# Optimization experiments

Measured on AMD Instinct MI355X. Metric: run time of the kernel, lower is better.

Reference implementation:

```python
import jax, jax.numpy as jnp
import numpy as np

D = 1024      # dim_input
H = 16        # n_heads
DH = 64       # dim_inner
S = 1024      # current_seq
M = 1024      # pre_seq (memory)
B = 2         # batch
SCALE = 1.0 / np.sqrt(DH)


def _rel_shift(x):
    # x: [S, J, B, H]; Transformer-XL relative shift
    s, j = x.shape[0], x.shape[1]
    zero = jnp.zeros((s, 1) + x.shape[2:], x.dtype)
    x = jnp.concatenate([zero, x], axis=1)            # [S, J+1, B, H]
    x = x.reshape((j + 1, s) + x.shape[2:])[1:]        # [J, S, B, H]
    return x.reshape((s, j) + x.shape[2:])             # [S, J, B, H]


def setup_inputs() -> dict:
    key = jax.random.key(0)
    ks = jax.random.split(key, 9)
    std = 1.0 / np.sqrt(D)
    return {
        "multi_head_input": jax.random.normal(ks[0], (S, B, D), jnp.float32),
        "position_emb": jax.random.normal(ks[1], (S + M, D), jnp.float32),
        "memory": jax.random.normal(ks[2], (M, B, D), jnp.float32),
        "u": jax.random.normal(ks[3], (H, DH), jnp.float32) * 0.02,
        "v": jax.random.normal(ks[4], (H, DH), jnp.float32) * 0.02,
        "W_kv": jax.random.normal(ks[5], (D, 2 * H * DH), jnp.float32) * std,
        "W_q": jax.random.normal(ks[6], (D, H * DH), jnp.float32) * std,
        "W_pos": jax.random.normal(ks[7], (D, H * DH), jnp.float32) * std,
        "W_out": jax.random.normal(ks[8], (H * DH, D), jnp.float32) * std,
    }


def reference(multi_head_input, position_emb, memory, u, v, W_kv, W_q, W_pos, W_out):
    s = multi_head_input.shape[0]
    m = memory.shape[0]
    b = multi_head_input.shape[1]
    x_mem = jnp.concatenate([memory, multi_head_input], axis=0)   # [M+S, B, D]
    kv = x_mem @ W_kv                                              # [M+S, B, 2*H*DH]
    k, val = jnp.split(kv, 2, axis=-1)
    k = k.reshape(m + s, b, H, DH)
    val = val.reshape(m + s, b, H, DH)
    q = (multi_head_input @ W_q).reshape(s, b, H, DH)              # [S, B, H, DH]

    # content term: (q + u) . k
    content = jnp.einsum('ibhd,jbhd->ijbh', q + u, k)              # [S, M+S, B, H]
    # position term: (q + v) . r, then rel_shift
    r = (position_emb @ W_pos).reshape(m + s, H, DH)               # [M+S, H, DH]
    pos = jnp.einsum('ibhd,jhd->ijbh', q + v, r)                   # [S, M+S, B, H]
    pos = _rel_shift(pos)

    attn = jax.nn.softmax((content + pos) * SCALE, axis=1)         # [S, M+S, B, H]
    out = jnp.einsum('ijbh,jbhd->ibhd', attn, val).reshape(s, b, H * DH)
    return out @ W_out                                             # [S, B, D]
```

## Files before the change

kernel.cpp:

```cpp
#include <hip/hip_runtime.h>
#include <hip/hip_bf16.h>
#include <hip/hip_fp16.h>
#include <math.h>

#define D    1024
#define H    16
#define DH   64
#define S    1024
#define M    1024
#define B    2
#define J    2048
#define SCALE 0.125f

typedef __attribute__((ext_vector_type(8))) short        bf16x8;
typedef __attribute__((ext_vector_type(4))) short        s16x4;
typedef __attribute__((ext_vector_type(8))) _Float16     h16x8;
typedef __attribute__((ext_vector_type(8))) unsigned short us8;
typedef __attribute__((ext_vector_type(4))) float        f32x4;

__device__ __forceinline__ short f2bs(float f) {
    __hip_bfloat16 t = __float2bfloat16(f);
    short r; __builtin_memcpy(&r, &t, 2); return r;
}
__device__ __forceinline__ unsigned short f2bf_fast(float f) {
    unsigned int u; __builtin_memcpy(&u, &f, 4);
    return (unsigned short)((u + 0x8000u) >> 16);
}

__device__ __forceinline__ void g2l16(const short* g, short* l) {
    __builtin_amdgcn_global_load_lds(
        (const __attribute__((address_space(1))) unsigned int*)g,
        (__attribute__((address_space(3))) unsigned int*)l, 16, 0, 0);
}

__global__ __launch_bounds__(256)
void prep(const float* __restrict__ mem, const float* __restrict__ x,
          const float* __restrict__ pemb,
          const float* __restrict__ Wkv, const float* __restrict__ Wq,
          const float* __restrict__ Wpos, const float* __restrict__ Wout,
          short* __restrict__ a_bf, short* __restrict__ p_bf,
          short* __restrict__ wkvt, short* __restrict__ wqt,
          short* __restrict__ wpt,  short* __restrict__ wot)
{
    __shared__ float t[64][65];
    int blk = blockIdx.x;
    const int tid = threadIdx.x;
    if (blk < 6144) {
        const int idx = (blk * 256 + tid) * 4;
        const int TWO_M = 2 * 1024 * 1024;
        float4 v; short* dst;
        if (idx < TWO_M)          { v = *(const float4*)(mem  + idx);           dst = a_bf + idx; }
        else if (idx < 2 * TWO_M) { v = *(const float4*)(x    + idx - TWO_M);   dst = a_bf + idx; }
        else                      { v = *(const float4*)(pemb + idx - 2*TWO_M); dst = p_bf + idx - 2*TWO_M; }
        s16x4 o = { f2bs(v.x), f2bs(v.y), f2bs(v.z), f2bs(v.w) };
        *(s16x4*)dst = o;
        return;
    }
    blk -= 6144;
    const float* src; short* dst; int N, t0;
    if (blk < 512)       { src = Wkv;  dst = wkvt; N = 2048; t0 = blk; }
    else if (blk < 768)  { src = Wq;   dst = wqt;  N = 1024; t0 = blk - 512; }
    else if (blk < 1024) { src = Wpos; dst = wpt;  N = 1024; t0 = blk - 768; }
    else                 { src = Wout; dst = wot;  N = 1024; t0 = blk - 1024; }
    const int ntn = N >> 6;
    const int k0 = (t0 / ntn) * 64, n0 = (t0 % ntn) * 64;
    #pragma unroll
    for (int e = tid; e < 4096; e += 256) {
        int r = e >> 6, c = e & 63;
        t[r][c] = src[(size_t)(k0 + r) * N + n0 + c];
    }
    __syncthreads();
    #pragma unroll
    for (int e = tid; e < 4096; e += 256) {
        int nr = e >> 6, kc = e & 63;
        dst[(size_t)(n0 + nr) * 1024 + k0 + kc] = f2bs(t[kc][nr]);
    }
}

__device__ __forceinline__ void gemm_core(const short* __restrict__ A,
                                          const short* __restrict__ Bt,
                                          short* As, short* Bs,
                                          int bm0, int bn0, int tid,
                                          f32x4 acc[4][4])
{
    const int w    = tid >> 6;
    const int wy   = w >> 1, wx = w & 1;
    const int lane = tid & 63;
    const int lm   = lane & 15;
    const int lq   = lane >> 4;

    for (int k0 = 0; k0 < 1024; k0 += 64) {
        const short* Ab = A  + (size_t)bm0 * 1024 + k0;
        const short* Bb = Bt + (size_t)bn0 * 1024 + k0;
        #pragma unroll
        for (int t = 0; t < 4; ++t) {
            int s = t * 256 + tid;
            int r = s >> 3, c = s & 7;
            int cg = c ^ (r & 7);
            g2l16(Ab + r * 1024 + cg * 8, As + s * 8);
            g2l16(Bb + r * 1024 + cg * 8, Bs + s * 8);
        }
        __syncthreads();
        #pragma unroll
        for (int kk = 0; kk < 2; ++kk) {
            bf16x8 af[4], bg[4];
            #pragma unroll
            for (int r4 = 0; r4 < 4; ++r4) {
                int ar = wy * 64 + r4 * 16 + lm;
                int kc = kk * 4 + lq;
                af[r4] = *(const bf16x8*)(As + ((ar << 3) + (kc ^ (ar & 7))) * 8);
            }
            #pragma unroll
            for (int c4 = 0; c4 < 4; ++c4) {
                int br = wx * 64 + c4 * 16 + lm;
                int kc = kk * 4 + lq;
                bg[c4] = *(const bf16x8*)(Bs + ((br << 3) + (kc ^ (br & 7))) * 8);
            }
            #pragma unroll
            for (int r4 = 0; r4 < 4; ++r4)
                #pragma unroll
                for (int c4 = 0; c4 < 4; ++c4)
                    acc[r4][c4] = __builtin_amdgcn_mfma_f32_16x16x32_bf16(
                        af[r4], bg[c4], acc[r4][c4], 0, 0, 0);
        }
        __syncthreads();
    }
}

__global__ __launch_bounds__(256)
void proj_fused(const short* __restrict__ a_bf, const short* __restrict__ p_bf,
                const short* __restrict__ wkvt, const short* __restrict__ wqt,
                const short* __restrict__ wpt,
                short* __restrict__ k_bf, short* __restrict__ vt_bf,
                short* __restrict__ qu_bf, short* __restrict__ qv_bf,
                short* __restrict__ r_bf,
                const float* __restrict__ uvec, const float* __restrict__ vvec)
{
    __shared__ __align__(16) short As[128 * 64];
    __shared__ __align__(16) short Bs[128 * 64];

    int blk = blockIdx.x;
    int mode, bx, by;
    const short *A, *Bt;
    if (blk < 512)      { bx = blk & 15; by = blk >> 4;
                          if (bx >= 8) { mode = 4; A = wkvt; Bt = a_bf; }
                          else         { mode = 0; A = a_bf; Bt = wkvt; } }
    else if (blk < 640) { int b2 = blk - 512; mode = 1; bx = b2 & 7; by = b2 >> 3;
                          A = a_bf + (size_t)2048 * 1024; Bt = wqt; }
    else                { int b3 = blk - 640; mode = 2; bx = b3 & 7; by = b3 >> 3;
                          A = p_bf; Bt = wpt; }
    const int bn0 = (mode == 4) ? by * 128 : bx * 128;
    const int bm0 = (mode == 4) ? bx * 128 : by * 128;
    const int tid = threadIdx.x;
    const int w = tid >> 6, wy = w >> 1, wx = w & 1;
    const int lane = tid & 63, lm = lane & 15, lq = lane >> 4;

    f32x4 acc[4][4];
    #pragma unroll
    for (int r = 0; r < 4; ++r)
        #pragma unroll
        for (int c = 0; c < 4; ++c) acc[r][c] = (f32x4){0.f, 0.f, 0.f, 0.f};

    gemm_core(A, Bt, As, Bs, bm0, bn0, tid, acc);

    #pragma unroll
    for (int r4 = 0; r4 < 4; ++r4) {
        #pragma unroll
        for (int c4 = 0; c4 < 4; ++c4) {
            const int n = bn0 + wx * 64 + c4 * 16 + lm;
            float ubias = 0.f, vbias = 0.f;
            if (mode == 1) { ubias = uvec[n]; vbias = vvec[n]; }
            #pragma unroll
            for (int reg = 0; reg < 4; ++reg) {
                const int m = bm0 + wy * 64 + r4 * 16 + lq * 4 + reg;
                const float val = acc[r4][c4][reg];
                if (mode == 0) {
                    int j = m >> 1, b = m & 1;
                    int h = n >> 6, d = n & 63;
                    k_bf[(((size_t)b * H + h) * J + j) * DH + d] = f2bs(val);
                } else if (mode == 4) {
                    int n2 = m - 1024, h = n2 >> 6, d = n2 & 63;
                    int j = n >> 1, b = n & 1;
                    vt_bf[(((size_t)b * H + h) * DH + d) * J + j] = f2bs(val);
                } else if (mode == 1) {
                    int i = m >> 1, b = m & 1;
                    int h = n >> 6, d = n & 63;
                    size_t o = (((size_t)b * H + h) * S + i) * DH + d;
                    qu_bf[o] = f2bs((val + ubias) * SCALE);
                    qv_bf[o] = f2bs((val + vbias) * SCALE);
                } else {
                    int h = n >> 6, d = n & 63;
                    r_bf[((size_t)h * J + m) * DH + d] = f2bs(val);
                }
            }
        }
    }
}

__global__ __launch_bounds__(256)
void gemm_out(const short* __restrict__ A, const short* __restrict__ Bt,
              float* __restrict__ out)
{
    __shared__ __align__(16) short As[128 * 64];
    __shared__ __align__(16) short Bs[128 * 64];
    const int bn0 = blockIdx.x * 128, bm0 = blockIdx.y * 128;
    const int tid = threadIdx.x;
    const int w = tid >> 6, wy = w >> 1, wx = w & 1;
    const int lane = tid & 63, lm = lane & 15, lq = lane >> 4;

    f32x4 acc[4][4];
    #pragma unroll
    for (int r = 0; r < 4; ++r)
        #pragma unroll
        for (int c = 0; c < 4; ++c) acc[r][c] = (f32x4){0.f, 0.f, 0.f, 0.f};

    gemm_core(A, Bt, As, Bs, bm0, bn0, tid, acc);

    #pragma unroll
    for (int r4 = 0; r4 < 4; ++r4)
        #pragma unroll
        for (int c4 = 0; c4 < 4; ++c4) {
            const int n = bn0 + wx * 64 + c4 * 16 + lm;
            #pragma unroll
            for (int reg = 0; reg < 4; ++reg) {
                const int m = bm0 + wy * 64 + r4 * 16 + lq * 4 + reg;
                out[(size_t)m * 1024 + n] = acc[r4][c4][reg];
            }
        }
}

__device__ __forceinline__ int sidx(int m, int c) {
    return (m << 10) + (c ^ (m << 3));
}

__global__ __launch_bounds__(512)
void attn_mfma(const short* __restrict__ qu_bf, const short* __restrict__ qv_bf,
               const short* __restrict__ k_bf,  const short* __restrict__ vt_bf,
               const short* __restrict__ r_bf,
               float* __restrict__ opart, float* __restrict__ ml)
{
    __shared__ unsigned short sc[32 * 1024];
    __half* sch = (__half*)sc;
    float*  scF = (float*)sc;

    const int bh  = blockIdx.x;
    const int it  = blockIdx.y;
    const int jh  = blockIdx.z;
    const int i0  = it * 32;
    const int cbeg = jh << 10, cend = cbeg + 1024;
    const int h   = bh & (H - 1);
    const int tid = threadIdx.x;
    const int w    = tid >> 6;
    const int lane = tid & 63;
    const int lm   = lane & 15;
    const int lq   = lane >> 4;
    const int slot = (it * 32 + bh) * 2 + jh;

    const short* qup0 = qu_bf + ((size_t)(bh * S + i0 + lm)) * DH + lq * 8;
    const short* qup1 = qup0 + 16 * DH;
    bf16x8 au00 = *(const bf16x8*)qup0,        au01 = *(const bf16x8*)(qup0 + 32);
    bf16x8 au10 = *(const bf16x8*)qup1,        au11 = *(const bf16x8*)(qup1 + 32);
    const short* qvp0 = qv_bf + ((size_t)(bh * S + i0 + lm)) * DH + lq * 8;
    const short* qvp1 = qvp0 + 16 * DH;
    bf16x8 av00 = *(const bf16x8*)qvp0,        av01 = *(const bf16x8*)(qvp0 + 32);
    bf16x8 av10 = *(const bf16x8*)qvp1,        av11 = *(const bf16x8*)(qvp1 + 32);
    int r1a = i0 + 1 + lm;  if (r1a > S - 1) r1a = S - 1;
    int r1b = i0 + 17 + lm; if (r1b > S - 1) r1b = S - 1;
    const short* qwp0 = qv_bf + ((size_t)(bh * S + r1a)) * DH + lq * 8;
    const short* qwp1 = qv_bf + ((size_t)(bh * S + r1b)) * DH + lq * 8;
    bf16x8 aw00 = *(const bf16x8*)qwp0,        aw01 = *(const bf16x8*)(qwp0 + 32);
    bf16x8 aw10 = *(const bf16x8*)qwp1,        aw11 = *(const bf16x8*)(qwp1 + 32);

    if (tid < 32) {
        int hole = i0 + tid + 1025;
        if (hole >= cbeg && hole < cend) sc[sidx(tid, hole - cbeg)] = 0;
    }

    const short* rbase = r_bf + (size_t)h * J * DH;

    {
        int tmp = cbeg + 977 - i0;
        int tlo = tmp > 0 ? ((tmp + 15) >> 4) : 0;
        int thi = (cend + 1022 - i0) >> 4; if (thi > 127) thi = 127;
        for (int t = tlo + w; t <= thi; t += 8) {
            const short* rp = rbase + (size_t)(t * 16 + lm) * DH + lq * 8;
            bf16x8 b0 = *(const bf16x8*)rp, b1 = *(const bf16x8*)(rp + 32);
            f32x4 c0 = {0.f,0.f,0.f,0.f}, c1 = {0.f,0.f,0.f,0.f};
            c0 = __builtin_amdgcn_mfma_f32_16x16x32_bf16(av00, b0, c0, 0, 0, 0);
            c1 = __builtin_amdgcn_mfma_f32_16x16x32_bf16(av10, b0, c1, 0, 0, 0);
            c0 = __builtin_amdgcn_mfma_f32_16x16x32_bf16(av01, b1, c0, 0, 0, 0);
            c1 = __builtin_amdgcn_mfma_f32_16x16x32_bf16(av11, b1, c1, 0, 0, 0);
            int cb = i0 + t * 16 + lm - 1023 - cbeg;
            int base = i0 + 16 * t - 1023;
            if (base >= cbeg && base + 46 < cend) {
                #pragma unroll
                for (int r = 0; r < 4; ++r) {
                    int m0 = lq * 4 + r, m1 = m0 + 16;
                    sch[sidx(m0, cb + m0)] = __float2half(c0[r]);
                    sch[sidx(m1, cb + m1)] = __float2half(c1[r]);
                }
            } else {
                #pragma unroll
                for (int r = 0; r < 4; ++r) {
                    int m0 = lq * 4 + r, m1 = m0 + 16;
                    int cA = cb + m0, cB = cb + m1;
                    if (cA >= 0 && cA < 1024) sch[sidx(m0, cA)] = __float2half(c0[r]);
                    if (cB >= 0 && cB < 1024) sch[sidx(m1, cB)] = __float2half(c1[r]);
                }
            }
        }
    }

    {
        int tmpw = cbeg - 1072 - i0;
        int tlw = tmpw > 0 ? ((tmpw + 15) >> 4) : 0;
        int thw = (cend - 1027 - i0) >> 4; if (thw > 127) thw = 127;
        for (int t = tlw + w; t <= thw; t += 8) {
            const short* rp = rbase + (size_t)(t * 16 + lm) * DH + lq * 8;
            bf16x8 b0 = *(const bf16x8*)rp, b1 = *(const bf16x8*)(rp + 32);
            f32x4 c0 = {0.f,0.f,0.f,0.f}, c1 = {0.f,0.f,0.f,0.f};
            c0 = __builtin_amdgcn_mfma_f32_16x16x32_bf16(aw00, b0, c0, 0, 0, 0);
            c1 = __builtin_amdgcn_mfma_f32_16x16x32_bf16(aw10, b0, c1, 0, 0, 0);
            c0 = __builtin_amdgcn_mfma_f32_16x16x32_bf16(aw01, b1, c0, 0, 0, 0);
            c1 = __builtin_amdgcn_mfma_f32_16x16x32_bf16(aw11, b1, c1, 0, 0, 0);
            int cb = i0 + t * 16 + lm + 1026 - cbeg;
            int base = i0 + 16 * t + 1026;
            if (base >= cbeg && base + 46 < cend) {
                #pragma unroll
                for (int r = 0; r < 4; ++r) {
                    int m0 = lq * 4 + r, m1 = m0 + 16;
                    sch[sidx(m0, cb + m0)] = __float2half(c0[r]);
                    sch[sidx(m1, cb + m1)] = __float2half(c1[r]);
                }
            } else {
                #pragma unroll
                for (int r = 0; r < 4; ++r) {
                    int m0 = lq * 4 + r, m1 = m0 + 16;
                    int cA = cb + m0, cB = cb + m1;
                    if (cA >= 0 && cA < 1024) sch[sidx(m0, cA)] = __float2half(c0[r]);
                    if (cB >= 0 && cB < 1024) sch[sidx(m1, cB)] = __float2half(c1[r]);
                }
            }
        }
    }

    const short* kbase = k_bf + (size_t)bh * J * DH;
    int tc0 = jh * 64 + w + 8 * ((it) & 7);
    int tc1 = jh * 64 + w + 8 * ((1 + it) & 7);
    const short* kp0 = kbase + (size_t)(tc0 * 16 + lm) * DH + lq * 8;
    const short* kp1 = kbase + (size_t)(tc1 * 16 + lm) * DH + lq * 8;
    bf16x8 kb0 = *(const bf16x8*)kp0, kb1 = *(const bf16x8*)(kp0 + 32);
    bf16x8 kb2 = *(const bf16x8*)kp1, kb3 = *(const bf16x8*)(kp1 + 32);
    __syncthreads();

    #pragma unroll 1
    for (int g = 0; g < 8; g += 2) {
        int t0 = jh * 64 + w + 8 * ((g + it) & 7);
        int t1 = jh * 64 + w + 8 * ((g + 1 + it) & 7);
        bf16x8 nb0, nb1, nb2, nb3;
        if (g + 2 < 8) {
            int u0 = jh * 64 + w + 8 * ((g + 2 + it) & 7);
            int u1 = jh * 64 + w + 8 * ((g + 3 + it) & 7);
            const short* np0 = kbase + (size_t)(u0 * 16 + lm) * DH + lq * 8;
            const short* np1 = kbase + (size_t)(u1 * 16 + lm) * DH + lq * 8;
            nb0 = *(const bf16x8*)np0; nb1 = *(const bf16x8*)(np0 + 32);
            nb2 = *(const bf16x8*)np1; nb3 = *(const bf16x8*)(np1 + 32);
        }
        int lc0 = t0 * 16 + lm - cbeg;
        int lc1 = t1 * 16 + lm - cbeg;
        f32x4 c0, c1, c2, c3;
        #pragma unroll
        for (int r = 0; r < 4; ++r) {
            c0[r] = __half2float(sch[sidx(lq * 4 + r, lc0)]);
            c1[r] = __half2float(sch[sidx(16 + lq * 4 + r, lc0)]);
            c2[r] = __half2float(sch[sidx(lq * 4 + r, lc1)]);
            c3[r] = __half2float(sch[sidx(16 + lq * 4 + r, lc1)]);
        }
        c0 = __builtin_amdgcn_mfma_f32_16x16x32_bf16(au00, kb0, c0, 0, 0, 0);
        c1 = __builtin_amdgcn_mfma_f32_16x16x32_bf16(au10, kb0, c1, 0, 0, 0);
        c2 = __builtin_amdgcn_mfma_f32_16x16x32_bf16(au00, kb2, c2, 0, 0, 0);
        c3 = __builtin_amdgcn_mfma_f32_16x16x32_bf16(au10, kb2, c3, 0, 0, 0);
        c0 = __builtin_amdgcn_mfma_f32_16x16x32_bf16(au01, kb1, c0, 0, 0, 0);
        c1 = __builtin_amdgcn_mfma_f32_16x16x32_bf16(au11, kb1, c1, 0, 0, 0);
        c2 = __builtin_amdgcn_mfma_f32_16x16x32_bf16(au01, kb3, c2, 0, 0, 0);
        c3 = __builtin_amdgcn_mfma_f32_16x16x32_bf16(au11, kb3, c3, 0, 0, 0);
        #pragma unroll
        for (int r = 0; r < 4; ++r) {
            sch[sidx(lq * 4 + r, lc0)]      = __float2half(c0[r]);
            sch[sidx(16 + lq * 4 + r, lc0)] = __float2half(c1[r]);
            sch[sidx(lq * 4 + r, lc1)]      = __float2half(c2[r]);
            sch[sidx(16 + lq * 4 + r, lc1)] = __float2half(c3[r]);
        }
        kb0 = nb0; kb1 = nb1; kb2 = nb2; kb3 = nb3;
    }

    const int dslice = w & 3, jq = w >> 2;
    const short* vtb = vt_bf + ((size_t)bh * DH + dslice * 16 + lm) * J + cbeg + jq * 512;
    bf16x8 cv0, cv1, cv2, cv3;
    {
        int j0 = (it & 3) * 128;
        cv0 = *(const bf16x8*)(vtb + j0 +  0 + lq * 8);
        cv1 = *(const bf16x8*)(vtb + j0 + 32 + lq * 8);
        cv2 = *(const bf16x8*)(vtb + j0 + 64 + lq * 8);
        cv3 = *(const bf16x8*)(vtb + j0 + 96 + lq * 8);
    }
    __syncthreads();

    {
        const int row = tid >> 4;
        const int cw  = (tid & 15) * 8;
        float ssum = 0.f;
        #pragma unroll
        for (int c = cw; c < 1024; c += 128) {
            int idx = sidx(row, c);
            h16x8 v = *(const h16x8*)(sc + idx);
            us8 e;
            #pragma unroll
            for (int k = 0; k < 8; ++k) {
                float ex = __builtin_amdgcn_exp2f((float)v[k] * 1.44269504f);
                ssum += ex;
                e[k] = f2bf_fast(ex);
            }
            *(us8*)(sc + idx) = e;
        }
        #pragma unroll
        for (int off = 1; off < 16; off <<= 1) ssum += __shfl_xor(ssum, off);
        if ((tid & 15) == 0) {
            ml[(size_t)slot * 64 + row * 2]     = 0.f;
            ml[(size_t)slot * 64 + row * 2 + 1] = ssum;
        }
    }
    __syncthreads();

    f32x4 pa0 = {0.f,0.f,0.f,0.f}, pa1 = {0.f,0.f,0.f,0.f};
    f32x4 pa2 = {0.f,0.f,0.f,0.f}, pa3 = {0.f,0.f,0.f,0.f};
    f32x4 pb0 = {0.f,0.f,0.f,0.f}, pb1 = {0.f,0.f,0.f,0.f};
    f32x4 pb2 = {0.f,0.f,0.f,0.f}, pb3 = {0.f,0.f,0.f,0.f};
    #pragma unroll 1
    for (int jo0 = 0; jo0 < 4; ++jo0) {
        bf16x8 nv0, nv1, nv2, nv3;
        if (jo0 < 3) {
            int jn = ((jo0 + 1 + it) & 3) * 128;
            nv0 = *(const bf16x8*)(vtb + jn +  0 + lq * 8);
            nv1 = *(const bf16x8*)(vtb + jn + 32 + lq * 8);
            nv2 = *(const bf16x8*)(vtb + jn + 64 + lq * 8);
            nv3 = *(const bf16x8*)(vtb + jn + 96 + lq * 8);
        }
        int j0 = ((jo0 + it) & 3) * 128;
        int lb = jq * 512 + j0;
        bf16x8 a0 = *(const bf16x8*)(sc + sidx(lm, lb +  0 + lq * 8));
        bf16x8 a1 = *(const bf16x8*)(sc + sidx(lm, lb + 32 + lq * 8));
        bf16x8 a2 = *(const bf16x8*)(sc + sidx(lm, lb + 64 + lq * 8));
        bf16x8 a3 = *(const bf16x8*)(sc + sidx(lm, lb + 96 + lq * 8));
        bf16x8 c0 = *(const bf16x8*)(sc + sidx(16 + lm, lb +  0 + lq * 8));
        bf16x8 c1 = *(const bf16x8*)(sc + sidx(16 + lm, lb + 32 + lq * 8));
        bf16x8 c2 = *(const bf16x8*)(sc + sidx(16 + lm, lb + 64 + lq * 8));
        bf16x8 c3 = *(const bf16x8*)(sc + sidx(16 + lm, lb + 96 + lq * 8));
        pa0 = __builtin_amdgcn_mfma_f32_16x16x32_bf16(a0, cv0, pa0, 0, 0, 0);
        pb0 = __builtin_amdgcn_mfma_f32_16x16x32_bf16(c0, cv0, pb0, 0, 0, 0);
        pa1 = __builtin_amdgcn_mfma_f32_16x16x32_bf16(a1, cv1, pa1, 0, 0, 0);
        pb1 = __builtin_amdgcn_mfma_f32_16x16x32_bf16(c1, cv1, pb1, 0, 0, 0);
        pa2 = __builtin_amdgcn_mfma_f32_16x16x32_bf16(a2, cv2, pa2, 0, 0, 0);
        pb2 = __builtin_amdgcn_mfma_f32_16x16x32_bf16(c2, cv2, pb2, 0, 0, 0);
        pa3 = __builtin_amdgcn_mfma_f32_16x16x32_bf16(a3, cv3, pa3, 0, 0, 0);
        pb3 = __builtin_amdgcn_mfma_f32_16x16x32_bf16(c3, cv3, pb3, 0, 0, 0);
        if (jo0 < 3) { cv0 = nv0; cv1 = nv1; cv2 = nv2; cv3 = nv3; }
    }
    __syncthreads();

    #pragma unroll
    for (int r = 0; r < 4; ++r) {
        int m0 = lq * 4 + r, m1 = m0 + 16;
        scF[jq * 2048 + m0 * 64 + dslice * 16 + lm] = pa0[r] + pa1[r] + pa2[r] + pa3[r];
        scF[jq * 2048 + m1 * 64 + dslice * 16 + lm] = pb0[r] + pb1[r] + pb2[r] + pb3[r];
    }
    __syncthreads();

    float* op = opart + (size_t)slot * 2048;
    #pragma unroll
    for (int e = tid; e < 2048; e += 512)
        op[e] = scF[e] + scF[2048 + e];
}

__global__ __launch_bounds__(256)
void attn_combine(const float* __restrict__ opart, const float* __restrict__ ml,
                  short* __restrict__ o_bf)
{
    const int blk = blockIdx.x;
    const int it = blk >> 5, bh = blk & 31;
    const int h = bh & 15, b = bh >> 4;
    __shared__ float wgt[32][2];
    const int tid = threadIdx.x;
    if (tid < 32) {
        float m0 = ml[(size_t)(blk * 2 + 0) * 64 + tid * 2];
        float l0 = ml[(size_t)(blk * 2 + 0) * 64 + tid * 2 + 1];
        float m1 = ml[(size_t)(blk * 2 + 1) * 64 + tid * 2];
        float l1 = ml[(size_t)(blk * 2 + 1) * 64 + tid * 2 + 1];
        float mx = fmaxf(m0, m1);
        float e0 = __expf(m0 - mx), e1 = __expf(m1 - mx);
        float inv = 1.0f / (e0 * l0 + e1 * l1);
        wgt[tid][0] = e0 * inv;
        wgt[tid][1] = e1 * inv;
    }
    __syncthreads();
    const float* p0 = opart + (size_t)(blk * 2 + 0) * 2048;
    const float* p1 = opart + (size_t)(blk * 2 + 1) * 2048;
    #pragma unroll
    for (int e = tid; e < 2048; e += 256) {
        int m = e >> 6, d = e & 63;
        float val = p0[e] * wgt[m][0] + p1[e] * wgt[m][1];
        o_bf[((size_t)(it * 32 + m) * B + b) * (H * DH) + h * DH + d] = f2bs(val);
    }
}

extern "C" void kernel_launch(void* const* d_in, const int* in_sizes, int n_in,
                              void* d_out, int out_size, void* d_ws, size_t ws_size,
                              hipStream_t stream)
{
    const float* x    = (const float*)d_in[0];
    const float* pemb = (const float*)d_in[1];
    const float* mem  = (const float*)d_in[2];
    const float* u    = (const float*)d_in[3];
    const float* v    = (const float*)d_in[4];
    const float* Wkv  = (const float*)d_in[5];
    const float* Wq   = (const float*)d_in[6];
    const float* Wpos = (const float*)d_in[7];
    const float* Wout = (const float*)d_in[8];
    float* out = (float*)d_out;

    char* p = (char*)d_ws;
    short* a_bf  = (short*)p; p += (size_t)4096 * 1024 * 2;
    short* p_bf  = (short*)p; p += (size_t)2048 * 1024 * 2;
    short* wkvt  = (short*)p; p += (size_t)2048 * 1024 * 2;
    short* wqt   = (short*)p; p += (size_t)1024 * 1024 * 2;
    short* wpt   = (short*)p; p += (size_t)1024 * 1024 * 2;
    short* wot   = (short*)p; p += (size_t)1024 * 1024 * 2;
    short* k_bf  = (short*)p; p += (size_t)B * H * J * DH * 2;
    short* vt_bf = (short*)p; p += (size_t)B * H * J * DH * 2;
    short* qu_bf = (short*)p; p += (size_t)B * H * S * DH * 2;
    short* qv_bf = (short*)p; p += (size_t)B * H * S * DH * 2;
    short* r_bf  = (short*)p; p += (size_t)H * J * DH * 2;
    short* o_bf  = (short*)p;

    float* opart = (float*)d_ws;
    float* ml    = (float*)((char*)d_ws + (size_t)16 * 1024 * 1024);

    prep<<<7424, 256, 0, stream>>>(mem, x, pemb, Wkv, Wq, Wpos, Wout,
                                   a_bf, p_bf, wkvt, wqt, wpt, wot);
    proj_fused<<<768, 256, 0, stream>>>(a_bf, p_bf, wkvt, wqt, wpt,
                                        k_bf, vt_bf, qu_bf, qv_bf, r_bf, u, v);
    attn_mfma<<<dim3(B * H, S / 32, 2), 512, 0, stream>>>(
        qu_bf, qv_bf, k_bf, vt_bf, r_bf, opart, ml);
    attn_combine<<<(S / 32) * B * H, 256, 0, stream>>>(opart, ml, o_bf);
    gemm_out<<<dim3(8, 16), 256, 0, stream>>>(o_bf, wot, out);
}
```

Before: 293.9 us.

## Fuse exp into PV MFMA loop with per-wave column ownership

Instead of a separate pass that exponentiates the score tile in shared memory and writes it back as bf16, each wave now takes its own 128-column slice. It exponentiates the fp16 scores in registers and feeds them straight into the P·V MFMAs, with each wave covering all four d-slices. This removes an LDS read-modify-write pass and one barrier. In exchange the per-wave partial outputs must be reduced across 8 waves through LDS, and row sums are written per wave and summed in the combine kernel, which is simplified because the row max is always zero.

Measured after the change: 295.5 us. No clear change (+0.6%).

```diff
diff --git a/kernel.cpp b/kernel.cpp
--- a/kernel.cpp
+++ b/kernel.cpp
@@ -237,9 +237,9 @@
 void attn_mfma(const short* __restrict__ qu_bf, const short* __restrict__ qv_bf,
                const short* __restrict__ k_bf,  const short* __restrict__ vt_bf,
                const short* __restrict__ r_bf,
-               float* __restrict__ opart, float* __restrict__ ml)
-{
-    __shared__ unsigned short sc[32 * 1024];
+               float* __restrict__ opart, float* __restrict__ lsum)
+{
+    __shared__ __align__(16) unsigned short sc[32 * 1024];
     __half* sch = (__half*)sc;
     float*  scF = (float*)sc;
 
@@ -393,114 +393,90 @@
         }
         kb0 = nb0; kb1 = nb1; kb2 = nb2; kb3 = nb3;
     }
-
-    const int dslice = w & 3, jq = w >> 2;
-    const short* vtb = vt_bf + ((size_t)bh * DH + dslice * 16 + lm) * J + cbeg + jq * 512;
-    bf16x8 cv0, cv1, cv2, cv3;
+    __syncthreads();
+
+    f32x4 acc[4][2];
+    #pragma unroll
+    for (int ds = 0; ds < 4; ++ds) {
+        acc[ds][0] = (f32x4){0.f, 0.f, 0.f, 0.f};
+        acc[ds][1] = (f32x4){0.f, 0.f, 0.f, 0.f};
+    }
+    float rs0 = 0.f, rs1 = 0.f;
+    #pragma unroll 1
+    for (int c = 0; c < 4; ++c) {
+        int jb = w * 128 + ((c + it) & 3) * 32;
+        h16x8 ra0 = *(const h16x8*)(sc + sidx(lm, jb + lq * 8));
+        h16x8 ra1 = *(const h16x8*)(sc + sidx(16 + lm, jb + lq * 8));
+        bf16x8 bv[4];
+        #pragma unroll
+        for (int ds = 0; ds < 4; ++ds)
+            bv[ds] = *(const bf16x8*)(vt_bf +
+                ((size_t)bh * DH + ds * 16 + lm) * J + cbeg + jb + lq * 8);
+        us8 pa, pb;
+        #pragma unroll
+        for (int k = 0; k < 8; ++k) {
+            float e0 = __builtin_amdgcn_exp2f((float)ra0[k] * 1.44269504f);
+            float e1 = __builtin_amdgcn_exp2f((float)ra1[k] * 1.44269504f);
+            rs0 += e0; rs1 += e1;
+            pa[k] = f2bf_fast(e0);
+            pb[k] = f2bf_fast(e1);
+        }
+        bf16x8 a0, a1;
+        __builtin_memcpy(&a0, &pa, 16);
+        __builtin_memcpy(&a1, &pb, 16);
+        #pragma unroll
+        for (int ds = 0; ds < 4; ++ds) {
+            acc[ds][0] = __builtin_amdgcn_mfma_f32_16x16x32_bf16(a0, bv[ds], acc[ds][0], 0, 0, 0);
+            acc[ds][1] = __builtin_amdgcn_mfma_f32_16x16x32_bf16(a1, bv[ds], acc[ds][1], 0, 0, 0);
+        }
+    }
+    rs0 += __shfl_xor(rs0, 16); rs0 += __shfl_xor(rs0, 32);
+    rs1 += __shfl_xor(rs1, 16); rs1 += __shfl_xor(rs1, 32);
+    if (lq == 0) {
+        lsum[(size_t)slot * 256 + w * 32 + lm]      = rs0;
+        lsum[(size_t)slot * 256 + w * 32 + 16 + lm] = rs1;
+    }
+    __syncthreads();
+
+    #pragma unroll
+    for (int ds = 0; ds < 4; ++ds)
+        #pragma unroll
+        for (int r = 0; r < 4; ++r) {
+            int m0 = lq * 4 + r, m1 = m0 + 16;
+            scF[w * 2048 + m0 * 64 + ds * 16 + lm] = acc[ds][0][r];
+            scF[w * 2048 + m1 * 64 + ds * 16 + lm] = acc[ds][1][r];
+        }
+    __syncthreads();
+
     {
-        int j0 = (it & 3) * 128;
-        cv0 = *(const bf16x8*)(vtb + j0 +  0 + lq * 8);
-        cv1 = *(const bf16x8*)(vtb + j0 + 32 + lq * 8);
-        cv2 = *(const bf16x8*)(vtb + j0 + 64 + lq * 8);
-        cv3 = *(const bf16x8*)(vtb + j0 + 96 + lq * 8);
-    }
-    __syncthreads();
-
-    {
-        const int row = tid >> 4;
-        const int cw  = (tid & 15) * 8;
-        float ssum = 0.f;
-        #pragma unroll
-        for (int c = cw; c < 1024; c += 128) {
-            int idx = sidx(row, c);
-            h16x8 v = *(const h16x8*)(sc + idx);
-            us8 e;
-            #pragma unroll
-            for (int k = 0; k < 8; ++k) {
-                float ex = __builtin_amdgcn_exp2f((float)v[k] * 1.44269504f);
-                ssum += ex;
-                e[k] = f2bf_fast(ex);
-            }
-            *(us8*)(sc + idx) = e;
-        }
-        #pragma unroll
-        for (int off = 1; off < 16; off <<= 1) ssum += __shfl_xor(ssum, off);
-        if ((tid & 15) == 0) {
-            ml[(size_t)slot * 64 + row * 2]     = 0.f;
-            ml[(size_t)slot * 64 + row * 2 + 1] = ssum;
-        }
-    }
-    __syncthreads();
-
-    f32x4 pa0 = {0.f,0.f,0.f,0.f}, pa1 = {0.f,0.f,0.f,0.f};
-    f32x4 pa2 = {0.f,0.f,0.f,0.f}, pa3 = {0.f,0.f,0.f,0.f};
-    f32x4 pb0 = {0.f,0.f,0.f,0.f}, pb1 = {0.f,0.f,0.f,0.f};
-    f32x4 pb2 = {0.f,0.f,0.f,0.f}, pb3 = {0.f,0.f,0.f,0.f};
-    #pragma unroll 1
-    for (int jo0 = 0; jo0 < 4; ++jo0) {
-        bf16x8 nv0, nv1, nv2, nv3;
-        if (jo0 < 3) {
-            int jn = ((jo0 + 1 + it) & 3) * 128;
-            nv0 = *(const bf16x8*)(vtb + jn +  0 + lq * 8);
-            nv1 = *(const bf16x8*)(vtb + jn + 32 + lq * 8);
-            nv2 = *(const bf16x8*)(vtb + jn + 64 + lq * 8);
-            nv3 = *(const bf16x8*)(vtb + jn + 96 + lq * 8);
-        }
-        int j0 = ((jo0 + it) & 3) * 128;
-        int lb = jq * 512 + j0;
-        bf16x8 a0 = *(const bf16x8*)(sc + sidx(lm, lb +  0 + lq * 8));
-        bf16x8 a1 = *(const bf16x8*)(sc + sidx(lm, lb + 32 + lq * 8));
-        bf16x8 a2 = *(const bf16x8*)(sc + sidx(lm, lb + 64 + lq * 8));
-        bf16x8 a3 = *(const bf16x8*)(sc + sidx(lm, lb + 96 + lq * 8));
-        bf16x8 c0 = *(const bf16x8*)(sc + sidx(16 + lm, lb +  0 + lq * 8));
-        bf16x8 c1 = *(const bf16x8*)(sc + sidx(16 + lm, lb + 32 + lq * 8));
-        bf16x8 c2 = *(const bf16x8*)(sc + sidx(16 + lm, lb + 64 + lq * 8));
-        bf16x8 c3 = *(const bf16x8*)(sc + sidx(16 + lm, lb + 96 + lq * 8));
-        pa0 = __builtin_amdgcn_mfma_f32_16x16x32_bf16(a0, cv0, pa0, 0, 0, 0);
-        pb0 = __builtin_amdgcn_mfma_f32_16x16x32_bf16(c0, cv0, pb0, 0, 0, 0);
-        pa1 = __builtin_amdgcn_mfma_f32_16x16x32_bf16(a1, cv1, pa1, 0, 0, 0);
-        pb1 = __builtin_amdgcn_mfma_f32_16x16x32_bf16(c1, cv1, pb1, 0, 0, 0);
-        pa2 = __builtin_amdgcn_mfma_f32_16x16x32_bf16(a2, cv2, pa2, 0, 0, 0);
-        pb2 = __builtin_amdgcn_mfma_f32_16x16x32_bf16(c2, cv2, pb2, 0, 0, 0);
-        pa3 = __builtin_amdgcn_mfma_f32_16x16x32_bf16(a3, cv3, pa3, 0, 0, 0);
-        pb3 = __builtin_amdgcn_mfma_f32_16x16x32_bf16(c3, cv3, pb3, 0, 0, 0);
-        if (jo0 < 3) { cv0 = nv0; cv1 = nv1; cv2 = nv2; cv3 = nv3; }
-    }
-    __syncthreads();
-
-    #pragma unroll
-    for (int r = 0; r < 4; ++r) {
-        int m0 = lq * 4 + r, m1 = m0 + 16;
-        scF[jq * 2048 + m0 * 64 + dslice * 16 + lm] = pa0[r] + pa1[r] + pa2[r] + pa3[r];
-        scF[jq * 2048 + m1 * 64 + dslice * 16 + lm] = pb0[r] + pb1[r] + pb2[r] + pb3[r];
-    }
-    __syncthreads();
-
-    float* op = opart + (size_t)slot * 2048;
-    #pragma unroll
-    for (int e = tid; e < 2048; e += 512)
-        op[e] = scF[e] + scF[2048 + e];
+        float* op = opart + (size_t)slot * 2048;
+        const int e = tid * 4;
+        float4 s = *(const float4*)(scF + e);
+        #pragma unroll
+        for (int r = 1; r < 8; ++r) {
+            float4 t = *(const float4*)(scF + r * 2048 + e);
+            s.x += t.x; s.y += t.y; s.z += t.z; s.w += t.w;
+        }
+        *(float4*)(op + e) = s;
+    }
 }
 
 __global__ __launch_bounds__(256)
-void attn_combine(const float* __restrict__ opart, const float* __restrict__ ml,
+void attn_combine(const float* __restrict__ opart, const float* __restrict__ lsum,
                   short* __restrict__ o_bf)
 {
     const int blk = blockIdx.x;
     const int it = blk >> 5, bh = blk & 31;
     const int h = bh & 15, b = bh >> 4;
-    __shared__ float wgt[32][2];
+    __shared__ float wgt[32];
     const int tid = threadIdx.x;
     if (tid < 32) {
-        float m0 = ml[(size_t)(blk * 2 + 0) * 64 + tid * 2];
-        float l0 = ml[(size_t)(blk * 2 + 0) * 64 + tid * 2 + 1];
-        float m1 = ml[(size_t)(blk * 2 + 1) * 64 + tid * 2];
-        float l1 = ml[(size_t)(blk * 2 + 1) * 64 + tid * 2 + 1];
-        float mx = fmaxf(m0, m1);
-        float e0 = __expf(m0 - mx), e1 = __expf(m1 - mx);
-        float inv = 1.0f / (e0 * l0 + e1 * l1);
-        wgt[tid][0] = e0 * inv;
-        wgt[tid][1] = e1 * inv;
+        float l = 0.f;
+        #pragma unroll
+        for (int wv = 0; wv < 8; ++wv)
+            l += lsum[(size_t)(blk * 2 + 0) * 256 + wv * 32 + tid]
+               + lsum[(size_t)(blk * 2 + 1) * 256 + wv * 32 + tid];
+        wgt[tid] = 1.0f / l;
     }
     __syncthreads();
     const float* p0 = opart + (size_t)(blk * 2 + 0) * 2048;
@@ -508,7 +484,7 @@
     #pragma unroll
     for (int e = tid; e < 2048; e += 256) {
         int m = e >> 6, d = e & 63;
-        float val = p0[e] * wgt[m][0] + p1[e] * wgt[m][1];
+        float val = (p0[e] + p1[e]) * wgt[m];
         o_bf[((size_t)(it * 32 + m) * B + b) * (H * DH) + h * DH + d] = f2bs(val);
     }
 }
@@ -543,14 +519,14 @@
     short* o_bf  = (short*)p;
 
     float* opart = (float*)d_ws;
-    float* ml    = (float*)((char*)d_ws + (size_t)16 * 1024 * 1024);
+    float* lsum  = (float*)((char*)d_ws + (size_t)16 * 1024 * 1024);
 
     prep<<<7424, 256, 0, stream>>>(mem, x, pemb, Wkv, Wq, Wpos, Wout,
                                    a_bf, p_bf, wkvt, wqt, wpt, wot);
     proj_fused<<<768, 256, 0, stream>>>(a_bf, p_bf, wkvt, wqt, wpt,
                                         k_bf, vt_bf, qu_bf, qv_bf, r_bf, u, v);
     attn_mfma<<<dim3(B * H, S / 32, 2), 512, 0, stream>>>(
-        qu_bf, qv_bf, k_bf, vt_bf, r_bf, opart, ml);
-    attn_combine<<<(S / 32) * B * H, 256, 0, stream>>>(opart, ml, o_bf);
+        qu_bf, qv_bf, k_bf, vt_bf, r_bf, opart, lsum);
+    attn_combine<<<(S / 32) * B * H, 256, 0, stream>>>(opart, lsum, o_bf);
     gemm_out<<<dim3(8, 16), 256, 0, stream>>>(o_bf, wot, out);
 }
```
